# Kernel tuning notes

Hardware: AMD Instinct MI355X
Metric: run time of the kernel (lower is better)

Reference implementation:

```python
import jax, jax.numpy as jnp
import numpy as np

CD_STEPS = 1

def _sample_binary(p, u):
    # relu(sign(p - u)): 1.0 where p > u else 0.0
    return (p > u).astype(p.dtype)

def setup_inputs() -> dict:
    key = jax.random.key(0)
    k_v, k_w, k_vb, k_uh, k_uv = jax.random.split(key, 5)
    B, V, H = 8192, 2048, 1024
    return {
        "v": jax.random.uniform(k_v, (B, V), dtype=jnp.float32),
        "w": jax.random.normal(k_w, (V, H), dtype=jnp.float32) * 0.01,
        "vb": jax.random.normal(k_vb, (V,), dtype=jnp.float32) * 0.01,
        "hb": jnp.zeros((H,), dtype=jnp.float32),
        "u_h": jax.random.uniform(k_uh, (CD_STEPS + 1, B, H), dtype=jnp.float32),
        "u_v": jax.random.uniform(k_uv, (CD_STEPS, B, V), dtype=jnp.float32),
    }

def reference(v, w, vb, hb, u_h, u_v):
    sig = jax.nn.sigmoid
    # mean-field forward
    h_p = sig(hb + v @ w)                     # [B,H]
    h_prediction = h_p
    v_prediction = sig(vb + h_p @ w.T)        # [B,V]
    reconstruction_error = jnp.mean(jnp.mean(jnp.abs(v - v_prediction), axis=1))
    # data statistics
    h = _sample_binary(h_p, u_h[0])           # [B,H]
    vb_data_grad = jnp.sum(v, axis=0)
    hb_data_grad = jnp.sum(h_p, axis=0)
    # sum_b outer(v_b, h_b) == v^T @ h (original materialized [B,V,H])
    w_data_grad = jnp.einsum('bv,bh->vh', v, h)
    # CD-k chain
    vk = v
    for k in range(CD_STEPS):
        vk = _sample_binary(sig(vb + h @ w.T), u_v[k])
        h = _sample_binary(sig(hb + vk @ w), u_h[k + 1])
    vb_model_grad = jnp.sum(vk, axis=0)
    hb_model_grad = jnp.sum(h, axis=0)
    w_model_grad = jnp.einsum('bv,bh->vh', vk, h)
    vb_grad = vb_model_grad - vb_data_grad
    hb_grad = hb_model_grad - hb_data_grad
    w_grad = w_model_grad - w_data_grad
    return h_prediction, reconstruction_error, w_grad, vb_grad, hb_grad
```

## Files before the change

kernel.cpp:

```cpp
#include <hip/hip_runtime.h>


typedef unsigned short u16;
typedef short s16x8 __attribute__((ext_vector_type(8)));
typedef float f32x4 __attribute__((ext_vector_type(4)));
typedef u16 u16x4 __attribute__((ext_vector_type(4)));
typedef u16 u16x8 __attribute__((ext_vector_type(8)));

constexpr int Bn = 8192, Vn = 2048, Hn = 1024;
constexpr size_t VH = (size_t)Vn * Hn;
constexpr size_t BH = (size_t)Bn * Hn;
constexpr size_t OUT_RECON = BH;
constexpr size_t OUT_WGRAD = OUT_RECON + 1;
constexpr size_t OUT_VBG   = OUT_WGRAD + VH;
constexpr size_t OUT_HBG   = OUT_VBG + Vn;

__device__ __forceinline__ u16 f2bf(float x) {
  union { float f; unsigned u; } a; a.f = x;
  unsigned r = a.u + 0x7FFFu + ((a.u >> 16) & 1u);
  return (u16)(r >> 16);
}
__device__ __forceinline__ float bf2f(u16 h) {
  union { unsigned u; float f; } a; a.u = ((unsigned)h) << 16;
  return a.f;
}
__device__ __forceinline__ float sigmoidf_(float x) {
  return 1.0f / (1.0f + __expf(-x));
}

using gptr_t = const unsigned int __attribute__((address_space(1)))*;
using lptr_t = unsigned int __attribute__((address_space(3)))*;

__device__ __forceinline__ void gload16(const u16* g, u16* l) {
  __builtin_amdgcn_global_load_lds((gptr_t)(unsigned long long)g,
                                   (lptr_t)(unsigned long long)l, 16, 0, 0);
}

__global__ void prep_all_k(const float* __restrict__ v, u16* __restrict__ vcat,
                           u16* __restrict__ vT, float* __restrict__ vbd_p,
                           const float* __restrict__ w, u16* __restrict__ w_cat,
                           u16* __restrict__ wTc) {
  __shared__ u16 tile16[64][68];
  __shared__ float cs[16][64];
  __shared__ float tile32[64][65];
  const int bx = blockIdx.x;
  const int t = threadIdx.x;
  if (bx < 4096) {
    const int b0 = (bx & 127) << 6, c0 = (bx >> 7) << 6;
    const int rg = t >> 4;
    const int cg = (t & 15) << 2;
    float ca[4] = {0.f, 0.f, 0.f, 0.f};
#pragma unroll
    for (int i = 0; i < 4; ++i) {
      int r = rg + 16 * i;
      f32x4 x = *(const f32x4*)&v[(size_t)(b0 + r) * Vn + c0 + cg];
      u16x4 hi, lo;
#pragma unroll
      for (int j = 0; j < 4; ++j) {
        hi[j] = f2bf(x[j]);
        lo[j] = f2bf(x[j] - bf2f(hi[j]));
        tile16[r][cg + j] = hi[j];
        ca[j] += x[j];
      }
      *(u16x4*)&vcat[(size_t)(b0 + r) * (2 * Vn) + c0 + cg] = hi;
      *(u16x4*)&vcat[(size_t)(b0 + r) * (2 * Vn) + Vn + c0 + cg] = lo;
    }
#pragma unroll
    for (int j = 0; j < 4; ++j) cs[rg][cg + j] = ca[j];
    __syncthreads();
    if (t < 64) {
      float s = 0.f;
#pragma unroll
      for (int k = 0; k < 16; ++k) s += cs[k][t];
      vbd_p[(size_t)(bx & 127) * Vn + c0 + t] = s;
    }
#pragma unroll
    for (int s2 = 0; s2 < 2; ++s2) {
      int c = t >> 2;
      int seg = (t & 3) + 4 * s2;
      u16x8 pk;
#pragma unroll
      for (int i = 0; i < 8; ++i) pk[i] = tile16[seg * 8 + i][c];
      *(u16x8*)&vT[(size_t)(c0 + c) * Bn + b0 + seg * 8] = pk;
    }
  } else {
    const int wb = bx - 4096;
    const int v0 = (wb & 31) << 6, h0 = (wb >> 5) << 6;
    const int c = t & 63, r = t >> 6;
    for (int rr = r; rr < 64; rr += 4) {
      float x = w[(size_t)(v0 + rr) * Hn + h0 + c];
      tile32[rr][c] = x;
      u16 hi = f2bf(x), lo = f2bf(x - bf2f(hi));
      w_cat[(size_t)(v0 + rr) * (2 * Hn) + h0 + c]      = hi;
      w_cat[(size_t)(v0 + rr) * (2 * Hn) + Hn + h0 + c] = lo;
    }
    __syncthreads();
    for (int rr = r; rr < 64; rr += 4) {
      float x = tile32[c][rr];
      u16 hi = f2bf(x), lo = f2bf(x - bf2f(hi));
      size_t ro = (size_t)(h0 + rr) * (2 * Vn);
      wTc[ro + v0 + c]      = hi;
      wTc[ro + Vn + v0 + c] = lo;
    }
  }
}

template <int M>
__global__ void epi_h_k(const float* __restrict__ p0, const float* __restrict__ p1,
                        const float* __restrict__ bias, const float* __restrict__ uni,
                        float* __restrict__ f32out, u16* __restrict__ hp_out,
                        u16* __restrict__ hbin_out, u16* __restrict__ tout,
                        float* __restrict__ colp) {
  __shared__ u16 tile[64][68];
  __shared__ float cs[16][64];
  const int b0 = blockIdx.x * 64, c0 = blockIdx.y * 64;
  const int t = threadIdx.x;
  const int rg = t >> 4, cg = (t & 15) << 2;
  float ca[4] = {0.f, 0.f, 0.f, 0.f};
#pragma unroll
  for (int i = 0; i < 4; ++i) {
    int r = rg + 16 * i;
    size_t e = (size_t)(b0 + r) * Hn + c0 + cg;
    f32x4 a = *(const f32x4*)&p0[e];
    f32x4 b = *(const f32x4*)&p1[e];
    f32x4 uu = *(const f32x4*)&uni[e];
    f32x4 hpv;
    u16x4 hb16, qv;
#pragma unroll
    for (int j = 0; j < 4; ++j) {
      float hp = sigmoidf_(a[j] + b[j] + bias[c0 + cg + j]);
      u16 qb = (hp > uu[j]) ? (u16)0x3F80 : (u16)0;
      tile[r][cg + j] = qb;
      if constexpr (M == 1) {
        hpv[j] = hp; hb16[j] = f2bf(hp); qv[j] = qb;
        ca[j] += hp;
      } else {
        ca[j] += (qb ? 1.f : 0.f);
      }
    }
    if constexpr (M == 1) {
      *(f32x4*)&f32out[e] = hpv;
      *(u16x4*)&hp_out[e] = hb16;
      *(u16x4*)&hbin_out[e] = qv;
    }
  }
#pragma unroll
  for (int j = 0; j < 4; ++j) cs[rg][cg + j] = ca[j];
  __syncthreads();
  if (t < 64) {
    float s = 0.f;
#pragma unroll
    for (int k = 0; k < 16; ++k) s += cs[k][t];
    colp[(size_t)blockIdx.x * Hn + c0 + t] = s;
  }
#pragma unroll
  for (int s2 = 0; s2 < 2; ++s2) {
    int c = t >> 2;
    int seg = (t & 3) + 4 * s2;
    u16x8 pk;
#pragma unroll
    for (int i = 0; i < 8; ++i) pk[i] = tile[seg * 8 + i][c];
    *(u16x8*)&tout[(size_t)(c0 + c) * Bn + b0 + seg * 8] = pk;
  }
}

template <int MODE>
__global__ __launch_bounds__(512) void gemm256(
    const u16* __restrict__ A, int lda, const u16* __restrict__ Bm, int ldb, int K,
    const float* __restrict__ bias, const float* __restrict__ uni,
    const float* __restrict__ aux, float* __restrict__ f32out,
    u16* __restrict__ bfout, const u16* __restrict__ aux16,
    float* __restrict__ redp, u16* __restrict__ tout, float* __restrict__ colp) {
  constexpr bool TRANS = (MODE == 4);
  __shared__ __align__(16) u16 smem[TRANS ? 67584 : 65536];
  const int t = threadIdx.x;
  const int lane = t & 63, wave = t >> 6;
  const int wr = (wave >> 2) << 7;
  const int wc = (wave & 3) << 6;
  int bidx = blockIdx.x, bidy = blockIdx.y, bidz = blockIdx.z;
  if constexpr (MODE == 3) {
    const int orig = blockIdx.x + (blockIdx.y << 3) + (blockIdx.z << 5);
    bidz = orig & 7;
    const int r = orig >> 3;
    bidx = r & 7;
    bidy = r >> 3;
  }
  const int bm = bidx << 8, bn = bidy << 8;
  int kbeg = 0;
  float* pout = f32out;
  if constexpr (MODE == 1 || MODE == 5) {
    kbeg = bidz * K;
    pout = (bidz == 0) ? f32out : redp;
  }
  if constexpr (MODE == 3) {
    size_t off = (size_t)bidz * (size_t)K;
    A += off;
    Bm += off;
    pout = ((bidz < 4) ? f32out : redp) + (size_t)(bidz & 3) * VH;
  }
  f32x4 acc[8][4] = {};
  const int sr = t >> 2;
  const int sc = (((t & 3) ^ ((t >> 3) & 3)) << 3);
  const u16* Ag  = A  + (size_t)(bm + sr) * lda + sc;
  const u16* Ag2 = Ag + (size_t)128 * lda;
  const u16* Bg  = Bm + (size_t)(bn + sr) * ldb + sc;
  const u16* Bg2 = Bg + (size_t)128 * ldb;
  const int fr = lane & 15, fg = lane >> 4;
  const int ga = ((fg ^ ((fr >> 1) & 3)) << 3);

  auto stage = [&](int kt) {
    const int k0 = kbeg + (kt << 5);
    int acol, bcol;
    if constexpr (MODE == 1) {
      acol = (k0 < 2048) ? k0 : k0 - 2048;
      bcol = (k0 < 4096) ? k0 : k0 - 4096;
    } else if constexpr (MODE == 4) { acol = k0 & 1023; bcol = k0; }
    else if constexpr (MODE == 5)   { acol = k0 & 2047; bcol = k0; }
    else                            { acol = k0;        bcol = k0; }
    const int pb = kt & 3;
    u16* ad = smem + pb * 8192 + wave * 512;
    u16* bd = smem + 32768 + pb * 8192 + wave * 512;
    gload16(Ag + acol, ad);
    gload16(Ag2 + acol, ad + 4096);
    gload16(Bg + bcol, bd);
    gload16(Bg2 + bcol, bd + 4096);
  };
  auto compute = [&](int kt) {
    const int pb = kt & 3;
    const u16* Ab = smem + pb * 8192;
    const u16* Bb = smem + 32768 + pb * 8192;
    s16x8 bf[4], af[4];
#pragma unroll
    for (int n = 0; n < 4; ++n)
      bf[n] = *(const s16x8*)&Bb[(wc + n * 16 + fr) * 32 + ga];
#pragma unroll
    for (int m = 0; m < 4; ++m)
      af[m] = *(const s16x8*)&Ab[(wr + m * 16 + fr) * 32 + ga];
    __builtin_amdgcn_s_setprio(1);
#pragma unroll
    for (int m = 0; m < 4; ++m)
#pragma unroll
      for (int n = 0; n < 4; ++n)
        acc[m][n] = __builtin_amdgcn_mfma_f32_16x16x32_bf16(af[m], bf[n], acc[m][n], 0, 0, 0);
    __builtin_amdgcn_s_setprio(0);
#pragma unroll
    for (int m = 0; m < 4; ++m)
      af[m] = *(const s16x8*)&Ab[(wr + (m + 4) * 16 + fr) * 32 + ga];
    __builtin_amdgcn_s_setprio(1);
#pragma unroll
    for (int m = 0; m < 4; ++m)
#pragma unroll
      for (int n = 0; n < 4; ++n)
        acc[m + 4][n] = __builtin_amdgcn_mfma_f32_16x16x32_bf16(af[m], bf[n], acc[m + 4][n], 0, 0, 0);
    __builtin_amdgcn_s_setprio(0);
  };
  auto pfl4 = [&](int ci) -> float {
    const int L = (ci << 9) + t;
    return uni[(size_t)(bm + (L >> 3)) * Vn + bn + ((L & 7) << 5)];
  };

  const int NT = K >> 5;
  const int pfbeg = NT - 8;
  stage(0); stage(1); stage(2);
  int T = 0;
  for (; T < NT - 3; ++T) {
    asm volatile("s_waitcnt vmcnt(8)" ::: "memory");
    __builtin_amdgcn_s_barrier();
    asm volatile("" ::: "memory");
    stage(T + 3);
    if constexpr (MODE == 4) {
      if (T >= pfbeg && T < pfbeg + 4) {
        float pfv = pfl4(T - pfbeg);
        asm volatile("" :: "v"(pfv));
      }
    }
    compute(T);
  }
  asm volatile("s_waitcnt vmcnt(8)" ::: "memory");
  __builtin_amdgcn_s_barrier();
  asm volatile("" ::: "memory");
  compute(T++);
  asm volatile("s_waitcnt vmcnt(4)" ::: "memory");
  __builtin_amdgcn_s_barrier();
  asm volatile("" ::: "memory");
  compute(T++);
  asm volatile("s_waitcnt vmcnt(0)" ::: "memory");
  __builtin_amdgcn_s_barrier();
  asm volatile("" ::: "memory");
  compute(T);

  constexpr int NC = (MODE == 4) ? Vn : Hn;
  const int fq = lane >> 4;

  if constexpr (MODE == 1 || MODE == 3 || MODE == 5) {
#pragma unroll
    for (int m = 0; m < 8; ++m)
#pragma unroll
      for (int n = 0; n < 4; ++n)
#pragma unroll
        for (int j = 0; j < 4; ++j) {
          int rl = wr + m * 16 + fq * 4 + j;
          int cl = wc + n * 16 + fr;
          pout[(size_t)(bm + rl) * NC + bn + cl] = acc[m][n][j];
        }
  }

  if constexpr (MODE == 4) {
    __syncthreads();
    float bcol[4];
#pragma unroll
    for (int n = 0; n < 4; ++n) bcol[n] = bias[bn + wc + n * 16 + fr];
    const size_t ebase = (size_t)(bm + wr + fq * 4) * NC + (bn + wc + fr);
    float ux[8][4];
    auto ld4 = [&](int ci, float* dst) {
      size_t e0 = ebase + (size_t)((ci >> 2) << 4) * NC + ((ci & 3) << 4);
      dst[0] = uni[e0];          dst[1] = uni[e0 + NC];
      dst[2] = uni[e0 + 2 * NC]; dst[3] = uni[e0 + 3 * NC];
    };
#pragma unroll
    for (int ci = 0; ci < 8; ++ci) ld4(ci, ux[ci]);
#pragma unroll
    for (int m = 0; m < 8; ++m)
#pragma unroll
      for (int n = 0; n < 4; ++n)
#pragma unroll
        for (int j = 0; j < 4; ++j)
          acc[m][n][j] = sigmoidf_(acc[m][n][j] + bcol[n]);
    float csum[4] = {0.f, 0.f, 0.f, 0.f};
#pragma unroll
    for (int ci = 0; ci < 32; ++ci) {
      const int m = ci >> 2, n = ci & 3;
      const int rl = wr + m * 16 + fq * 4;
      const int cl = wc + n * 16 + fr;
#pragma unroll
      for (int j = 0; j < 4; ++j) {
        u16 qb = (acc[m][n][j] > ux[ci & 7][j]) ? (u16)0x3F80 : (u16)0;
        smem[(rl + j) * 264 + cl] = qb;
        csum[n] += (qb ? 1.f : 0.f);
      }
      if (ci < 24) ld4(ci + 8, ux[ci & 7]);
    }
#pragma unroll
    for (int n = 0; n < 4; ++n) {
      float s = csum[n];
      s += __shfl_xor(s, 16);
      s += __shfl_xor(s, 32);
      if (fq == 0)
        colp[(size_t)(blockIdx.x * 2 + (wr >> 7)) * NC + (bn + wc + n * 16 + fr)] = s;
    }
    __syncthreads();
#pragma unroll
    for (int it = 0; it < 16; ++it) {
      int id = t + (it << 9);
      int r = id >> 5;
      int c0 = (id & 31) << 3;
      u16x8 pk = *(const u16x8*)&smem[r * 264 + c0];
      *(u16x8*)&bfout[(size_t)(bm + r) * NC + bn + c0] = pk;
    }
#pragma unroll
    for (int it = 0; it < 4; ++it) {
      int id = t + (it << 9);
      int c = id & 255;
      int q = id >> 8;
#pragma unroll
      for (int i8 = 0; i8 < 4; ++i8) {
        u16x8 pk;
#pragma unroll
        for (int i2 = 0; i2 < 8; ++i2)
          pk[i2] = smem[(q * 32 + i8 * 8 + i2) * 264 + c];
        *(u16x8*)&tout[(size_t)(bn + c) * Bn + bm + q * 32 + i8 * 8] = pk;
      }
    }
  }
}

__global__ __launch_bounds__(512) void g23_k(
    const u16* __restrict__ A2, const u16* __restrict__ B2,
    const u16* __restrict__ aux16, const float* __restrict__ bias2,
    float* __restrict__ redp2,
    const u16* __restrict__ A3, const u16* __restrict__ B3,
    float* __restrict__ out30, float* __restrict__ out34) {
  __shared__ __align__(16) u16 smem[65536];
  const int t = threadIdx.x;
  const int lane = t & 63, wave = t >> 6;
  const int wr = (wave >> 2) << 7;
  const int wc = (wave & 3) << 6;
  const int flat = blockIdx.x;
  const bool isG2 = (flat < 256);
  int bidx, bidy, bidz = 0;
  const u16 *Abase, *Bbase;
  int lda, ldb;
  if (isG2) {
    bidx = flat & 31; bidy = flat >> 5;
    Abase = A2; Bbase = B2; lda = Hn; ldb = 2 * Hn;
  } else {
    const int orig = flat - 256;
    bidz = orig & 7;
    const int rr = orig >> 3;
    bidx = rr & 7; bidy = rr >> 3;
    Abase = A3 + (size_t)bidz * 1024;
    Bbase = B3 + (size_t)bidz * 1024;
    lda = Bn; ldb = Bn;
  }
  const int bm = bidx << 8, bn = bidy << 8;
  f32x4 acc[8][4] = {};
  const int sr = t >> 2;
  const int sc = (((t & 3) ^ ((t >> 3) & 3)) << 3);
  const u16* Ag  = Abase + (size_t)(bm + sr) * lda + sc;
  const u16* Ag2 = Ag + (size_t)128 * lda;
  const u16* Bg  = Bbase + (size_t)(bn + sr) * ldb + sc;
  const u16* Bg2 = Bg + (size_t)128 * ldb;
  const int fr = lane & 15, fg = lane >> 4;
  const int ga = ((fg ^ ((fr >> 1) & 3)) << 3);

  auto stage = [&](int kt) {
    const int k0 = kt << 5;
    const int pb = kt & 3;
    u16* ad = smem + pb * 8192 + wave * 512;
    u16* bd = smem + 32768 + pb * 8192 + wave * 512;
    gload16(Ag + k0, ad);
    gload16(Ag2 + k0, ad + 4096);
    gload16(Bg + k0, bd);
    gload16(Bg2 + k0, bd + 4096);
  };
  auto compute = [&](int kt) {
    const int pb = kt & 3;
    const u16* Ab = smem + pb * 8192;
    const u16* Bb = smem + 32768 + pb * 8192;
    s16x8 bf[4], af[4];
#pragma unroll
    for (int n = 0; n < 4; ++n)
      bf[n] = *(const s16x8*)&Bb[(wc + n * 16 + fr) * 32 + ga];
#pragma unroll
    for (int m = 0; m < 4; ++m)
      af[m] = *(const s16x8*)&Ab[(wr + m * 16 + fr) * 32 + ga];
    __builtin_amdgcn_s_setprio(1);
#pragma unroll
    for (int m = 0; m < 4; ++m)
#pragma unroll
      for (int n = 0; n < 4; ++n)
        acc[m][n] = __builtin_amdgcn_mfma_f32_16x16x32_bf16(af[m], bf[n], acc[m][n], 0, 0, 0);
    __builtin_amdgcn_s_setprio(0);
#pragma unroll
    for (int m = 0; m < 4; ++m)
      af[m] = *(const s16x8*)&Ab[(wr + (m + 4) * 16 + fr) * 32 + ga];
    __builtin_amdgcn_s_setprio(1);
#pragma unroll
    for (int m = 0; m < 4; ++m)
#pragma unroll
      for (int n = 0; n < 4; ++n)
        acc[m + 4][n] = __builtin_amdgcn_mfma_f32_16x16x32_bf16(af[m], bf[n], acc[m + 4][n], 0, 0, 0);
    __builtin_amdgcn_s_setprio(0);
  };
  auto pfl2 = [&](int ci) -> unsigned {
    const int L = (ci << 9) + t;
    return (unsigned)aux16[(size_t)(bm + (L >> 2)) * 4096 + bn + ((L & 3) << 6)];
  };

  constexpr int NT = 32;
  stage(0); stage(1); stage(2);
  int T = 0;
  for (; T < NT - 3; ++T) {
    asm volatile("s_waitcnt vmcnt(8)" ::: "memory");
    __builtin_amdgcn_s_barrier();
    asm volatile("" ::: "memory");
    stage(T + 3);
    if (isG2 && T >= NT - 8 && T < NT - 6) {
      unsigned pfv = pfl2(T - (NT - 8));
      asm volatile("" :: "v"(pfv));
    }
    compute(T);
  }
  asm volatile("s_waitcnt vmcnt(8)" ::: "memory");
  __builtin_amdgcn_s_barrier();
  asm volatile("" ::: "memory");
  compute(T++);
  asm volatile("s_waitcnt vmcnt(4)" ::: "memory");
  __builtin_amdgcn_s_barrier();
  asm volatile("" ::: "memory");
  compute(T++);
  asm volatile("s_waitcnt vmcnt(0)" ::: "memory");
  __builtin_amdgcn_s_barrier();
  asm volatile("" ::: "memory");
  compute(T);

  const int fq = lane >> 4;
  if (isG2) {
    float bcol[4];
#pragma unroll
    for (int n = 0; n < 4; ++n) bcol[n] = bias2[bn + wc + n * 16 + fr];
    const size_t ebase = (size_t)(bm + wr + fq * 4) * 4096 + (bn + wc + fr);
    float ax[8][4];
    auto ld4 = [&](int ci, float* dst) {
      size_t e0 = ebase + (size_t)((ci >> 2) << 4) * 4096 + ((ci & 3) << 4);
      dst[0] = bf2f(aux16[e0]);            dst[1] = bf2f(aux16[e0 + 4096]);
      dst[2] = bf2f(aux16[e0 + 2 * 4096]); dst[3] = bf2f(aux16[e0 + 3 * 4096]);
    };
#pragma unroll
    for (int ci = 0; ci < 8; ++ci) ld4(ci, ax[ci]);
#pragma unroll
    for (int m = 0; m < 8; ++m)
#pragma unroll
      for (int n = 0; n < 4; ++n)
#pragma unroll
        for (int j = 0; j < 4; ++j)
          acc[m][n][j] = sigmoidf_(acc[m][n][j] + bcol[n]);
    float lsum = 0.f;
#pragma unroll
    for (int ci = 0; ci < 32; ++ci) {
      const int m = ci >> 2, n = ci & 3;
#pragma unroll
      for (int j = 0; j < 4; ++j) lsum += fabsf(ax[ci & 7][j] - acc[m][n][j]);
      if (ci < 24) ld4(ci + 8, ax[ci & 7]);
    }
#pragma unroll
    for (int off = 32; off > 0; off >>= 1) lsum += __shfl_down(lsum, off);
    __syncthreads();
    float* redlds = (float*)smem;
    if (lane == 0) redlds[wave] = lsum;
    __syncthreads();
    if (t == 0) {
      float s = 0.f;
#pragma unroll
      for (int wv = 0; wv < 8; ++wv) s += redlds[wv];
      redp2[(size_t)bidy * 32 + bidx] = s;
    }
  } else {
    float* pout = ((bidz < 4) ? out30 : out34) + (size_t)(bidz & 3) * VH;
#pragma unroll
    for (int m = 0; m < 8; ++m)
#pragma unroll
      for (int n = 0; n < 4; ++n)
#pragma unroll
        for (int j = 0; j < 4; ++j) {
          int rl = wr + m * 16 + fq * 4 + j;
          int cl = wc + n * 16 + fr;
          pout[(size_t)(bm + rl) * Hn + bn + cl] = acc[m][n][j];
        }
  }
}

__global__ void reduce8_k(const float* __restrict__ p, float* __restrict__ out) {
  size_t e = ((size_t)blockIdx.x * 256 + threadIdx.x) * 4;
  f32x4 r = {};
#pragma unroll
  for (int z = 0; z < 8; ++z) r += *(const f32x4*)&p[(size_t)z * VH + e];
  out[e + 0] = r[0]; out[e + 1] = r[1]; out[e + 2] = r[2]; out[e + 3] = r[3];
}

__global__ void tail_k(const float* __restrict__ pa, const float* __restrict__ pb,
                       const float* __restrict__ sums, float* __restrict__ out) {
  const int b = blockIdx.x;
  float* outw = out + OUT_WGRAD;
  if (b < 2048) {
    size_t e = ((size_t)b * 256 + threadIdx.x) * 4;
    f32x4 r = {};
#pragma unroll
    for (int z = 0; z < 4; ++z) r += *(const f32x4*)&pa[(size_t)z * VH + e];
#pragma unroll
    for (int z = 0; z < 4; ++z) r += *(const f32x4*)&pb[(size_t)z * VH + e];
    float s0 = outw[e + 0], s1 = outw[e + 1], s2 = outw[e + 2], s3 = outw[e + 3];
    outw[e + 0] = r[0] - s0; outw[e + 1] = r[1] - s1;
    outw[e + 2] = r[2] - s2; outw[e + 3] = r[3] - s3;
  } else {
    const int i = (b - 2048) * 256 + threadIdx.x;
    const float* recon_p = sums;
    const float* vbd = sums + 1024;
    const float* hbd = vbd + 128 * 2048;
    const float* vbm = hbd + 128 * 1024;
    const float* hbm = vbm + 128 * 2048;
    if (i < 2048) {
      float d = 0.f, m = 0.f;
      for (int k = 0; k < 128; ++k) d += vbd[k * 2048 + i];
      for (int k = 0; k < 64; ++k)  m += vbm[k * 2048 + i];
      out[OUT_VBG + i] = m - d;
    }
    if (i < 1024) {
      float d = 0.f, m = 0.f;
      for (int k = 0; k < 128; ++k) { d += hbd[k * 1024 + i]; m += hbm[k * 1024 + i]; }
      out[OUT_HBG + i] = m - d;
    }
    if (i == 0) {
      float s = 0.f;
      for (int k = 0; k < 256; ++k) s += recon_p[k];
      out[OUT_RECON] = s * (1.0f / 16777216.0f);
    }
  }
}

extern "C" void kernel_launch(void* const* d_in, const int* in_sizes, int n_in,
                              void* d_out, int out_size, void* d_ws, size_t ws_size,
                              hipStream_t stream) {
  (void)in_sizes; (void)n_in; (void)out_size;
  const float* v   = (const float*)d_in[0];
  const float* w   = (const float*)d_in[1];
  const float* vb  = (const float*)d_in[2];
  const float* hb  = (const float*)d_in[3];
  const float* u_h = (const float*)d_in[4];
  const float* u_v = (const float*)d_in[5];
  float* out = (float*)d_out;
  char* ws = (char*)d_ws;
  if (ws_size < 204734464ULL) return;

  float* sums    = (float*)ws;
  float* recon_p = sums;
  float* vbd_p   = sums + 1024;
  float* hbd_p   = vbd_p + 128 * 2048;
  float* vbm_p   = hbd_p + 128 * 1024;
  float* hbm_p   = vbm_p + 128 * 2048;
  char* p = ws + 3407872;
  u16* v_cat  = (u16*)p;  p += (size_t)Bn * 2 * Vn * 2;
  u16* wT_cat = (u16*)p;  p += (size_t)Hn * 2 * Vn * 2;
  u16* w_cat  = (u16*)p;  p += (size_t)Vn * 2 * Hn * 2;
  u16* h_p    = (u16*)p;  p += BH * 2;
  u16* hbin   = (u16*)p;  p += BH * 2;
  u16* vT     = (u16*)p;  p += (size_t)Vn * Bn * 2;
  u16* hT     = (u16*)p;  p += (size_t)Hn * Bn * 2;
  float* big  = (float*)p;
  u16* vk   = v_cat;
  u16* vkT  = vT;
  u16* h2T  = hT;
  float* vcat_f = (float*)v_cat;
  float* hpbuf  = (float*)h_p;
  float* outW   = out + OUT_WGRAD;

  prep_all_k<<<4608, 256, 0, stream>>>(v, v_cat, vT, vbd_p, w, w_cat, wT_cat);
  gemm256<1><<<dim3(32, 4, 2), 512, 0, stream>>>(
      v_cat, 2 * Vn, wT_cat, 2 * Vn, 3072, nullptr, nullptr, nullptr,
      out, nullptr, nullptr, big, nullptr, nullptr);
  epi_h_k<1><<<dim3(128, 16), 256, 0, stream>>>(
      out, big, hb, u_h, out, h_p, hbin, hT, hbd_p);
  g23_k<<<512, 512, 0, stream>>>(
      h_p, w_cat, v_cat, vb, recon_p,
      vT, hT, vcat_f, vcat_f + 4 * VH);
  reduce8_k<<<2048, 256, 0, stream>>>(vcat_f, outW);
  gemm256<4><<<dim3(32, 8), 512, 0, stream>>>(
      hbin, Hn, w_cat, 2 * Hn, 2 * Hn, vb, u_v, nullptr,
      nullptr, vk, nullptr, nullptr, vkT, vbm_p);
  gemm256<5><<<dim3(32, 4, 2), 512, 0, stream>>>(
      vk, Vn, wT_cat, 2 * Vn, 2048, nullptr, nullptr, nullptr,
      hpbuf, nullptr, nullptr, big, nullptr, nullptr);
  epi_h_k<5><<<dim3(128, 16), 256, 0, stream>>>(
      hpbuf, big, hb, u_h + BH, nullptr, nullptr, nullptr, h2T, hbm_p);
  gemm256<3><<<dim3(Vn / 256, Hn / 256, 8), 512, 0, stream>>>(
      vkT, Bn, h2T, Bn, 1024, nullptr, nullptr, nullptr,
      hpbuf, nullptr, nullptr, big, nullptr, nullptr);
  tail_k<<<2056, 256, 0, stream>>>(hpbuf, big, sums, out);
}
```

Baseline: 498.6 us.

## Interleave split A/B global staging with MFMA halves in GEMM main loops

Restructures the K-loop of both GEMM kernels so the A and B tile loads for stage kt+3 are issued separately, between the two MFMA half-blocks. The waitcnt and barrier now sit mid-iteration, and the epilogue iterations are folded into one loop with conditional waits. The aim is to spread global-load issue across compute, hide LDS read latency and shorten barrier stalls, at the cost of two barriers per iteration and tighter ordering on the LDS buffers.

```diff
diff --git a/kernel.cpp b/kernel.cpp
--- a/kernel.cpp
+++ b/kernel.cpp
@@ -208,34 +208,62 @@
   const int fr = lane & 15, fg = lane >> 4;
   const int ga = ((fg ^ ((fr >> 1) & 3)) << 3);
 
-  auto stage = [&](int kt) {
+  auto acolf = [&](int k0) -> int {
+    if constexpr (MODE == 1)      return (k0 < 2048) ? k0 : k0 - 2048;
+    else if constexpr (MODE == 4) return k0 & 1023;
+    else if constexpr (MODE == 5) return k0 & 2047;
+    else                          return k0;
+  };
+  auto bcolf = [&](int k0) -> int {
+    if constexpr (MODE == 1) return (k0 < 4096) ? k0 : k0 - 4096;
+    else                     return k0;
+  };
+  auto stageA = [&](int kt) {
     const int k0 = kbeg + (kt << 5);
-    int acol, bcol;
-    if constexpr (MODE == 1) {
-      acol = (k0 < 2048) ? k0 : k0 - 2048;
-      bcol = (k0 < 4096) ? k0 : k0 - 4096;
-    } else if constexpr (MODE == 4) { acol = k0 & 1023; bcol = k0; }
-    else if constexpr (MODE == 5)   { acol = k0 & 2047; bcol = k0; }
-    else                            { acol = k0;        bcol = k0; }
-    const int pb = kt & 3;
-    u16* ad = smem + pb * 8192 + wave * 512;
-    u16* bd = smem + 32768 + pb * 8192 + wave * 512;
+    const int acol = acolf(k0);
+    u16* ad = smem + (kt & 3) * 8192 + wave * 512;
     gload16(Ag + acol, ad);
     gload16(Ag2 + acol, ad + 4096);
+  };
+  auto stageB = [&](int kt) {
+    const int k0 = kbeg + (kt << 5);
+    const int bcol = bcolf(k0);
+    u16* bd = smem + 32768 + (kt & 3) * 8192 + wave * 512;
     gload16(Bg + bcol, bd);
     gload16(Bg2 + bcol, bd + 4096);
   };
-  auto compute = [&](int kt) {
+  auto pfl4 = [&](int ci) -> float {
+    const int L = (ci << 9) + t;
+    return uni[(size_t)(bm + (L >> 3)) * Vn + bn + ((L & 7) << 5)];
+  };
+
+  const int NT = K >> 5;
+  const int pfbeg = NT - 8;
+  stageA(0); stageB(0); stageA(1); stageB(1); stageA(2); stageB(2);
+  asm volatile("s_waitcnt vmcnt(8)" ::: "memory");
+  __builtin_amdgcn_s_barrier();
+  asm volatile("" ::: "memory");
+  s16x8 bf[4], af[4];
+  for (int kt = 0; kt < NT; ++kt) {
     const int pb = kt & 3;
     const u16* Ab = smem + pb * 8192;
     const u16* Bb = smem + 32768 + pb * 8192;
-    s16x8 bf[4], af[4];
+    const bool st = (kt < NT - 3);
 #pragma unroll
     for (int n = 0; n < 4; ++n)
       bf[n] = *(const s16x8*)&Bb[(wc + n * 16 + fr) * 32 + ga];
 #pragma unroll
     for (int m = 0; m < 4; ++m)
       af[m] = *(const s16x8*)&Ab[(wr + m * 16 + fr) * 32 + ga];
+    if (st) stageA(kt + 3);
+    if constexpr (MODE == 4) {
+      if (kt >= pfbeg && kt < pfbeg + 4) {
+        float pfv = pfl4(kt - pfbeg);
+        asm volatile("" :: "v"(pfv));
+      }
+    }
+    __builtin_amdgcn_s_barrier();
+    asm volatile("" ::: "memory");
     __builtin_amdgcn_s_setprio(1);
 #pragma unroll
     for (int m = 0; m < 4; ++m)
@@ -246,6 +274,16 @@
 #pragma unroll
     for (int m = 0; m < 4; ++m)
       af[m] = *(const s16x8*)&Ab[(wr + (m + 4) * 16 + fr) * 32 + ga];
+    if (st) stageB(kt + 3);
+    if (kt < NT - 3) {
+      asm volatile("s_waitcnt vmcnt(8)" ::: "memory");
+    } else if (kt == NT - 3) {
+      asm volatile("s_waitcnt vmcnt(4)" ::: "memory");
+    } else if (kt == NT - 2) {
+      asm volatile("s_waitcnt vmcnt(0)" ::: "memory");
+    }
+    __builtin_amdgcn_s_barrier();
+    asm volatile("" ::: "memory");
     __builtin_amdgcn_s_setprio(1);
 #pragma unroll
     for (int m = 0; m < 4; ++m)
@@ -253,41 +291,7 @@
       for (int n = 0; n < 4; ++n)
         acc[m + 4][n] = __builtin_amdgcn_mfma_f32_16x16x32_bf16(af[m], bf[n], acc[m + 4][n], 0, 0, 0);
     __builtin_amdgcn_s_setprio(0);
-  };
-  auto pfl4 = [&](int ci) -> float {
-    const int L = (ci << 9) + t;
-    return uni[(size_t)(bm + (L >> 3)) * Vn + bn + ((L & 7) << 5)];
-  };
-
-  const int NT = K >> 5;
-  const int pfbeg = NT - 8;
-  stage(0); stage(1); stage(2);
-  int T = 0;
-  for (; T < NT - 3; ++T) {
-    asm volatile("s_waitcnt vmcnt(8)" ::: "memory");
-    __builtin_amdgcn_s_barrier();
-    asm volatile("" ::: "memory");
-    stage(T + 3);
-    if constexpr (MODE == 4) {
-      if (T >= pfbeg && T < pfbeg + 4) {
-        float pfv = pfl4(T - pfbeg);
-        asm volatile("" :: "v"(pfv));
-      }
-    }
-    compute(T);
-  }
-  asm volatile("s_waitcnt vmcnt(8)" ::: "memory");
-  __builtin_amdgcn_s_barrier();
-  asm volatile("" ::: "memory");
-  compute(T++);
-  asm volatile("s_waitcnt vmcnt(4)" ::: "memory");
-  __builtin_amdgcn_s_barrier();
-  asm volatile("" ::: "memory");
-  compute(T++);
-  asm volatile("s_waitcnt vmcnt(0)" ::: "memory");
-  __builtin_amdgcn_s_barrier();
-  asm volatile("" ::: "memory");
-  compute(T);
+  }
 
   constexpr int NC = (MODE == 4) ? Vn : Hn;
   const int fq = lane >> 4;
@@ -413,27 +417,45 @@
   const int fr = lane & 15, fg = lane >> 4;
   const int ga = ((fg ^ ((fr >> 1) & 3)) << 3);
 
-  auto stage = [&](int kt) {
-    const int k0 = kt << 5;
-    const int pb = kt & 3;
-    u16* ad = smem + pb * 8192 + wave * 512;
-    u16* bd = smem + 32768 + pb * 8192 + wave * 512;
-    gload16(Ag + k0, ad);
-    gload16(Ag2 + k0, ad + 4096);
-    gload16(Bg + k0, bd);
-    gload16(Bg2 + k0, bd + 4096);
-  };
-  auto compute = [&](int kt) {
+  auto stageA = [&](int kt) {
+    u16* ad = smem + (kt & 3) * 8192 + wave * 512;
+    gload16(Ag + (kt << 5), ad);
+    gload16(Ag2 + (kt << 5), ad + 4096);
+  };
+  auto stageB = [&](int kt) {
+    u16* bd = smem + 32768 + (kt & 3) * 8192 + wave * 512;
+    gload16(Bg + (kt << 5), bd);
+    gload16(Bg2 + (kt << 5), bd + 4096);
+  };
+  auto pfl2 = [&](int ci) -> unsigned {
+    const int L = (ci << 9) + t;
+    return (unsigned)aux16[(size_t)(bm + (L >> 2)) * 4096 + bn + ((L & 3) << 6)];
+  };
+
+  constexpr int NT = 32;
+  stageA(0); stageB(0); stageA(1); stageB(1); stageA(2); stageB(2);
+  asm volatile("s_waitcnt vmcnt(8)" ::: "memory");
+  __builtin_amdgcn_s_barrier();
+  asm volatile("" ::: "memory");
+  s16x8 bf[4], af[4];
+  for (int kt = 0; kt < NT; ++kt) {
     const int pb = kt & 3;
     const u16* Ab = smem + pb * 8192;
     const u16* Bb = smem + 32768 + pb * 8192;
-    s16x8 bf[4], af[4];
+    const bool st = (kt < NT - 3);
 #pragma unroll
     for (int n = 0; n < 4; ++n)
       bf[n] = *(const s16x8*)&Bb[(wc + n * 16 + fr) * 32 + ga];
 #pragma unroll
     for (int m = 0; m < 4; ++m)
       af[m] = *(const s16x8*)&Ab[(wr + m * 16 + fr) * 32 + ga];
+    if (st) stageA(kt + 3);
+    if (isG2 && kt >= NT - 8 && kt < NT - 6) {
+      unsigned pfv = pfl2(kt - (NT - 8));
+      asm volatile("" :: "v"(pfv));
+    }
+    __builtin_amdgcn_s_barrier();
+    asm volatile("" ::: "memory");
     __builtin_amdgcn_s_setprio(1);
 #pragma unroll
     for (int m = 0; m < 4; ++m)
@@ -444,6 +466,16 @@
 #pragma unroll
     for (int m = 0; m < 4; ++m)
       af[m] = *(const s16x8*)&Ab[(wr + (m + 4) * 16 + fr) * 32 + ga];
+    if (st) stageB(kt + 3);
+    if (kt < NT - 3) {
+      asm volatile("s_waitcnt vmcnt(8)" ::: "memory");
+    } else if (kt == NT - 3) {
+      asm volatile("s_waitcnt vmcnt(4)" ::: "memory");
+    } else if (kt == NT - 2) {
+      asm volatile("s_waitcnt vmcnt(0)" ::: "memory");
+    }
+    __builtin_amdgcn_s_barrier();
+    asm volatile("" ::: "memory");
     __builtin_amdgcn_s_setprio(1);
 #pragma unroll
     for (int m = 0; m < 4; ++m)
@@ -451,38 +483,7 @@
       for (int n = 0; n < 4; ++n)
         acc[m + 4][n] = __builtin_amdgcn_mfma_f32_16x16x32_bf16(af[m], bf[n], acc[m + 4][n], 0, 0, 0);
     __builtin_amdgcn_s_setprio(0);
-  };
-  auto pfl2 = [&](int ci) -> unsigned {
-    const int L = (ci << 9) + t;
-    return (unsigned)aux16[(size_t)(bm + (L >> 2)) * 4096 + bn + ((L & 3) << 6)];
-  };
-
-  constexpr int NT = 32;
-  stage(0); stage(1); stage(2);
-  int T = 0;
-  for (; T < NT - 3; ++T) {
-    asm volatile("s_waitcnt vmcnt(8)" ::: "memory");
-    __builtin_amdgcn_s_barrier();
-    asm volatile("" ::: "memory");
-    stage(T + 3);
-    if (isG2 && T >= NT - 8 && T < NT - 6) {
-      unsigned pfv = pfl2(T - (NT - 8));
-      asm volatile("" :: "v"(pfv));
-    }
-    compute(T);
-  }
-  asm volatile("s_waitcnt vmcnt(8)" ::: "memory");
-  __builtin_amdgcn_s_barrier();
-  asm volatile("" ::: "memory");
-  compute(T++);
-  asm volatile("s_waitcnt vmcnt(4)" ::: "memory");
-  __builtin_amdgcn_s_barrier();
-  asm volatile("" ::: "memory");
-  compute(T++);
-  asm volatile("s_waitcnt vmcnt(0)" ::: "memory");
-  __builtin_amdgcn_s_barrier();
-  asm volatile("" ::: "memory");
-  compute(T);
+  }
 
   const int fq = lane >> 4;
   if (isG2) {
```

Result: no change. 493.8 us (median of 2 runs) (-1.0%).
